# Optimization experiments

Measured on AMD Instinct MI355X. Metric: run time of the kernel, lower is better.

## Reference

```python
import jax, jax.numpy as jnp
import numpy as np

IN_F = 4096
OUT_F = 4096
PACKED_IN = IN_F // 16  # 16 ternary values per int32 (2 bits each)
TOKENS = 8192


def _pack(vals_int32):
    # vals_int32: [out, packed_in, 16] with entries in {0,1,2}
    shifts = (jnp.arange(16, dtype=jnp.int32) * 2)
    return jnp.sum(vals_int32 << shifts, axis=-1).astype(jnp.int32)


def _unpack_weight(packed, scale, in_features):
    # packed: [out, packed_in] int32 -> fp32 weight [out, in_features]
    shifts = (jnp.arange(16, dtype=jnp.int32) * 2)
    vals = (packed[:, :, None] >> shifts) & 3           # [out, packed_in, 16]
    w = vals.reshape(packed.shape[0], -1)[:, :in_features]
    return (w.astype(jnp.float32) - 1.0) * scale


def setup_inputs() -> dict:
    key = jax.random.key(0)
    k1, k2 = jax.random.split(key)
    x = jax.random.normal(k1, (TOKENS, IN_F), dtype=jnp.float32)
    # mapped ternary values in {0,1,2} (i.e. w_ternary + 1), packed 2-bit
    mapped = jax.random.randint(k2, (OUT_F, PACKED_IN, 16), 0, 3, dtype=jnp.int32)
    packed_weight = _pack(mapped)
    scale = jnp.float32(0.02)
    return {"x": x, "packed_weight": packed_weight, "scale": scale}


def reference(x, packed_weight, scale):
    # dequantize ternary weight
    w = _unpack_weight(packed_weight, scale, IN_F)      # [out, in]
    # abs-max activation scaling along the last dim
    x_scale = jnp.clip(jnp.max(jnp.abs(x), axis=-1, keepdims=True), 1e-5, None)
    x_scaled = x / x_scale
    out = jnp.einsum('ti,oi->to', x_scaled, w)          # F.linear (no bias)
    return out * x_scale
```

## Files before the change

### kernel.cpp

```cpp
#include <hip/hip_runtime.h>
#include <math.h>

typedef __attribute__((ext_vector_type(4)))  int   i32x4;
typedef __attribute__((ext_vector_type(16))) int   i32x16;
typedef __attribute__((ext_vector_type(4)))  float f32x4;

namespace {
constexpr int IN_F   = 4096;
constexpr int OUT_F  = 4096;
constexpr int TOKENS = 8192;
constexpr int PACKED = IN_F / 16;

constexpr int BM   = 256;
constexpr int BN   = 256;
constexpr int BK   = 128;
constexpr int NTHR = 512;
constexpr int NT   = IN_F / BK;

constexpr size_t XQ_BYTES = (size_t)TOKENS * IN_F;
constexpr size_t XS_BYTES = (size_t)TOKENS * 4;
constexpr size_t BQ_OFF   = XQ_BYTES + XS_BYTES;
constexpr size_t BQ_BYTES = (size_t)PACKED * OUT_F * 16;
constexpr size_t WS_NEED  = BQ_OFF + BQ_BYTES;
}

__device__ __forceinline__ i32x4 unpack16(unsigned w) {
  i32x4 r;
#pragma unroll
  for (int g = 0; g < 4; ++g) {
    unsigned t = (w >> (8 * g)) & 0xFFu;
    unsigned s = (t | (t << 6) | (t << 12) | (t << 18)) & 0x03030303u;
    r[g] = (int)((((s | 0x80808080u) - 0x01010101u) ^ 0x80808080u));
  }
  return r;
}

__global__ __launch_bounds__(256)
void prep(const float* __restrict__ X, signed char* __restrict__ XQ,
          float* __restrict__ XS, const unsigned* __restrict__ PW,
          signed char* __restrict__ BQ) {
  if (blockIdx.x < TOKENS / 4) {
    const int row  = blockIdx.x * 4 + (threadIdx.x >> 6);
    const int lane = threadIdx.x & 63;
    const float* xr = X + (size_t)row * IN_F;

    f32x4 v[16];
    float m = 0.f;
#pragma unroll
    for (int c = 0; c < 16; ++c) {
      v[c] = *(const f32x4*)(xr + c * 256 + lane * 4);
      m = fmaxf(m, fmaxf(fmaxf(fabsf(v[c].x), fabsf(v[c].y)),
                         fmaxf(fabsf(v[c].z), fabsf(v[c].w))));
    }
#pragma unroll
    for (int off = 32; off; off >>= 1) m = fmaxf(m, __shfl_xor(m, off, 64));
    m = fmaxf(m, 1e-5f);
    const float r = 127.f / m;

#pragma unroll
    for (int c = 0; c < 16; ++c) {
      int q0 = (int)rintf(v[c].x * r);
      int q1 = (int)rintf(v[c].y * r);
      int q2 = (int)rintf(v[c].z * r);
      int q3 = (int)rintf(v[c].w * r);
      unsigned d = (q0 & 255) | ((q1 & 255) << 8) | ((q2 & 255) << 16) | ((q3 & 255) << 24);
      *(unsigned*)(XQ + (size_t)row * IN_F + c * 256 + lane * 4) = d;
    }
    if (lane == 0) XS[row] = m;
  } else {
    const int g = (blockIdx.x - TOKENS / 4) * 256 + threadIdx.x;
    const int c = g >> 12;
    const int n = g & 4095;
    i32x4 u = unpack16(PW[(size_t)n * PACKED + c]);
    *(i32x4*)(BQ + ((size_t)c * OUT_F + n) * 16) = u;
  }
}


#define STAGE_A(BUF_, KT_)                                                      \
  {                                                                             \
    _Pragma("unroll")                                                           \
    for (int rb = 0; rb < 4; ++rb) {                                            \
      const signed char* src =                                                  \
          XQ + (size_t)(m0 + rb * 64 + lane) * IN_F + (KT_) * BK + w * 16;      \
      signed char* dst = lA + (BUF_) * 32768 + w * 4096 + rb * 1024;            \
      __builtin_amdgcn_global_load_lds(                                         \
          (const __attribute__((address_space(1))) void*)src,                   \
          (__attribute__((address_space(3))) void*)dst, 16, 0, 0);              \
    }                                                                           \
  }

#define STAGE_B(BUF_, KT_)                                                      \
  {                                                                             \
    _Pragma("unroll")                                                           \
    for (int j = 0; j < 4; ++j) {                                               \
      const signed char* src =                                                  \
          BQ + ((size_t)((KT_) * 8 + w) * OUT_F + n0 + j * 64 + lane) * 16;     \
      signed char* dst = lB + (BUF_) * 32768 + w * 4096 + j * 1024;             \
      __builtin_amdgcn_global_load_lds(                                         \
          (const __attribute__((address_space(1))) void*)src,                   \
          (__attribute__((address_space(3))) void*)dst, 16, 0, 0);              \
    }                                                                           \
  }

#define PHASE(KS_, BUF_)                                                        \
  {                                                                             \
    i32x4 afr[4], bfr[2];                                                       \
    _Pragma("unroll")                                                           \
    for (int mf = 0; mf < 4; ++mf)                                              \
      afr[mf] = *(const i32x4*)(lA + (BUF_) * 32768 + ((KS_) * 2 + h) * 4096 +  \
                                (wm * 128 + mf * 32 + l31) * 16);               \
    _Pragma("unroll")                                                           \
    for (int nf = 0; nf < 2; ++nf)                                              \
      bfr[nf] = *(const i32x4*)(lB + (BUF_) * 32768 + ((KS_) * 2 + h) * 4096 +  \
                                (wn * 64 + nf * 32 + l31) * 16);                \
    __builtin_amdgcn_s_setprio(1);                                              \
    _Pragma("unroll")                                                           \
    for (int mf = 0; mf < 4; ++mf) {                                            \
      acc[mf][0] = __builtin_amdgcn_mfma_i32_32x32x32_i8(afr[mf], bfr[0],       \
                                                         acc[mf][0], 0, 0, 0);  \
      acc[mf][1] = __builtin_amdgcn_mfma_i32_32x32x32_i8(afr[mf], bfr[1],       \
                                                         acc[mf][1], 0, 0, 0);  \
    }                                                                           \
    __builtin_amdgcn_s_setprio(0);                                              \
  }

#define TILE(KT_, CUR_, NXT_, PF_)                                              \
  {                                                                             \
    if (PF_) STAGE_A(NXT_, (KT_) + 1);                                          \
    PHASE(0, CUR_)                                                              \
    if (PF_) STAGE_B(NXT_, (KT_) + 1);                                          \
    PHASE(1, CUR_)                                                              \
    PHASE(2, CUR_)                                                              \
    PHASE(3, CUR_)                                                              \
    asm volatile("s_waitcnt vmcnt(0)" ::: "memory");                            \
    __builtin_amdgcn_s_barrier();                                               \
  }

__global__ __launch_bounds__(NTHR, 2)
void gemm_i8(const signed char* __restrict__ XQ, const signed char* __restrict__ BQ,
             const float* __restrict__ XS, const float* __restrict__ SC,
             float* __restrict__ OUT) {
  __shared__ signed char lA[2 * 32768];
  __shared__ signed char lB[2 * 32768];

  const int tid  = threadIdx.x;
  const int lane = tid & 63;
  const int w    = tid >> 6;
  const int wm   = w >> 2;
  const int wn   = w & 3;
  const int l31  = lane & 31;
  const int h    = lane >> 5;

  const int orig = blockIdx.y * gridDim.x + blockIdx.x;
  const int xcd  = orig & 7;
  const int idx  = orig >> 3;
  const int m0   = (idx >> 1) * BM;
  const int n0   = (xcd * 2 + (idx & 1)) * BN;

  i32x16 acc[4][2];
#pragma unroll
  for (int mf = 0; mf < 4; ++mf)
#pragma unroll
    for (int nf = 0; nf < 2; ++nf)
      acc[mf][nf] = (i32x16)(0);

  STAGE_A(0, 0);
  STAGE_B(0, 0);
  asm volatile("s_waitcnt vmcnt(0)" ::: "memory");
  __builtin_amdgcn_s_barrier();

  for (int kt = 0; kt < NT - 2; kt += 2) {
    TILE(kt,     0, 1, true);
    TILE(kt + 1, 1, 0, true);
  }
  TILE(NT - 2, 0, 1, true);
  TILE(NT - 1, 1, 0, false);

  const float sc = SC[0] / 127.f;
#pragma unroll
  for (int mf = 0; mf < 4; ++mf) {
    float fs[16];
#pragma unroll
    for (int r = 0; r < 16; ++r) {
      const int mm = m0 + wm * 128 + mf * 32 + 4 * h + (r & 3) + 8 * (r >> 2);
      fs[r] = sc * XS[mm];
    }
#pragma unroll
    for (int nf = 0; nf < 2; ++nf) {
      const int ncol = n0 + wn * 64 + nf * 32 + l31;
#pragma unroll
      for (int r = 0; r < 16; ++r) {
        const int mm = m0 + wm * 128 + mf * 32 + 4 * h + (r & 3) + 8 * (r >> 2);
        OUT[(size_t)mm * OUT_F + ncol] = (float)acc[mf][nf][r] * fs[r];
      }
    }
  }
}

__global__ __launch_bounds__(256, 2)
void gemm_i8_pw(const signed char* __restrict__ XQ, const unsigned* __restrict__ PW,
                const float* __restrict__ XS, const float* __restrict__ SC,
                float* __restrict__ OUT) {
  __shared__ signed char lA[256 * 128];

  const int tid  = threadIdx.x;
  const int lane = tid & 63;
  const int w    = tid >> 6;
  const int wm   = w >> 1;
  const int wn   = w & 1;
  const int l31  = lane & 31;
  const int h    = lane >> 5;

  const int m0 = blockIdx.y * 256;
  const int n0 = blockIdx.x * 128;

  i32x16 acc[4][2];
#pragma unroll
  for (int mf = 0; mf < 4; ++mf)
#pragma unroll
    for (int nf = 0; nf < 2; ++nf)
      acc[mf][nf] = (i32x16)(0);

  const unsigned* pb0 = PW + (size_t)(n0 + wn * 64 + 0 * 32 + l31) * PACKED;
  const unsigned* pb1 = PW + (size_t)(n0 + wn * 64 + 1 * 32 + l31) * PACKED;

  for (int kt = 0; kt < IN_F / 128; ++kt) {
#pragma unroll
    for (int cc = 0; cc < 2; ++cc) {
      const int c = w * 2 + cc;
#pragma unroll
      for (int rb = 0; rb < 4; ++rb) {
        const signed char* src =
            XQ + (size_t)(m0 + rb * 64 + lane) * IN_F + kt * 128 + c * 16;
        signed char* dst = lA + c * 4096 + rb * 1024;
        __builtin_amdgcn_global_load_lds(
            (const __attribute__((address_space(1))) void*)src,
            (__attribute__((address_space(3))) void*)dst, 16, 0, 0);
      }
    }

    unsigned bw0[4], bw1[4];
#pragma unroll
    for (int ks = 0; ks < 4; ++ks) {
      bw0[ks] = pb0[kt * 8 + ks * 2 + h];
      bw1[ks] = pb1[kt * 8 + ks * 2 + h];
    }

    __syncthreads();

#pragma unroll
    for (int ks = 0; ks < 4; ++ks) {
      i32x4 bfr0 = unpack16(bw0[ks]);
      i32x4 bfr1 = unpack16(bw1[ks]);
      i32x4 afr[4];
#pragma unroll
      for (int mf = 0; mf < 4; ++mf)
        afr[mf] = *(const i32x4*)(lA + (ks * 2 + h) * 4096 +
                                  (wm * 128 + mf * 32 + l31) * 16);
#pragma unroll
      for (int mf = 0; mf < 4; ++mf) {
        acc[mf][0] = __builtin_amdgcn_mfma_i32_32x32x32_i8(afr[mf], bfr0, acc[mf][0], 0, 0, 0);
        acc[mf][1] = __builtin_amdgcn_mfma_i32_32x32x32_i8(afr[mf], bfr1, acc[mf][1], 0, 0, 0);
      }
    }
    __syncthreads();
  }

  const float sc = SC[0] / 127.f;
#pragma unroll
  for (int mf = 0; mf < 4; ++mf) {
    float fs[16];
#pragma unroll
    for (int r = 0; r < 16; ++r) {
      const int mm = m0 + wm * 128 + mf * 32 + 4 * h + (r & 3) + 8 * (r >> 2);
      fs[r] = sc * XS[mm];
    }
#pragma unroll
    for (int nf = 0; nf < 2; ++nf) {
      const int ncol = n0 + wn * 64 + nf * 32 + l31;
#pragma unroll
      for (int r = 0; r < 16; ++r) {
        const int mm = m0 + wm * 128 + mf * 32 + 4 * h + (r & 3) + 8 * (r >> 2);
        OUT[(size_t)mm * OUT_F + ncol] = (float)acc[mf][nf][r] * fs[r];
      }
    }
  }
}

extern "C" void kernel_launch(void* const* d_in, const int* in_sizes, int n_in,
                              void* d_out, int out_size, void* d_ws, size_t ws_size,
                              hipStream_t stream) {
  const float*    x  = (const float*)d_in[0];
  const unsigned* pw = (const unsigned*)d_in[1];
  const float*    sc = (const float*)d_in[2];
  float*          out = (float*)d_out;

  signed char* xq = (signed char*)d_ws;
  float*       xs = (float*)((char*)d_ws + XQ_BYTES);

  if (ws_size >= WS_NEED) {
    signed char* bq = (signed char*)d_ws + BQ_OFF;
    prep<<<dim3(TOKENS / 4 + OUT_F * PACKED / 256), dim3(256), 0, stream>>>(
        x, xq, xs, pw, bq);
    dim3 grid(OUT_F / BN, TOKENS / BM);
    gemm_i8<<<grid, dim3(NTHR), 0, stream>>>(xq, bq, xs, sc, out);
  } else {
    prep<<<dim3(TOKENS / 4), dim3(256), 0, stream>>>(x, xq, xs, pw, nullptr);
    dim3 grid(OUT_F / 128, TOKENS / 256);
    gemm_i8_pw<<<grid, dim3(256), 0, stream>>>(xq, pw, xs, sc, out);
  }
}
```

Before: 397.0 us.

## Switch int8 GEMM to triple-buffered LDS pipeline with BK=64

Halves the K tile to 64 and replaces the double-buffered LDS scheme with three rotating buffers, prefetching two tiles ahead and waiting only on the older tile's loads via vmcnt(4). The aim is to keep more global-to-LDS traffic in flight and hide memory latency behind the MFMA work. Occupancy hint drops from 2 to 1 block per CU. The trade-off is twice as many barriers per K and less work per barrier interval.

```diff
diff --git a/kernel.cpp b/kernel.cpp
--- a/kernel.cpp
+++ b/kernel.cpp
@@ -13,7 +13,7 @@
 
 constexpr int BM   = 256;
 constexpr int BN   = 256;
-constexpr int BK   = 128;
+constexpr int BK   = 64;
 constexpr int NTHR = 512;
 constexpr int NT   = IN_F / BK;
 
@@ -77,42 +77,44 @@
 }
 
 
-#define STAGE_A(BUF_, KT_)                                                      \
+#define STAGE_A(BUFO_, KT_)                                                     \
   {                                                                             \
     _Pragma("unroll")                                                           \
-    for (int rb = 0; rb < 4; ++rb) {                                            \
+    for (int j = 0; j < 2; ++j) {                                               \
+      const int idx  = tid + j * 512;            \
       const signed char* src =                                                  \
-          XQ + (size_t)(m0 + rb * 64 + lane) * IN_F + (KT_) * BK + w * 16;      \
-      signed char* dst = lA + (BUF_) * 32768 + w * 4096 + rb * 1024;            \
+          XQ + (size_t)(m0 + (idx & 255)) * IN_F + (KT_) * BK + (idx >> 8) * 16;\
+      signed char* dst = lA + (BUFO_) + (w * 64 + j * 512) * 16;                \
       __builtin_amdgcn_global_load_lds(                                         \
           (const __attribute__((address_space(1))) void*)src,                   \
           (__attribute__((address_space(3))) void*)dst, 16, 0, 0);              \
     }                                                                           \
   }
 
-#define STAGE_B(BUF_, KT_)                                                      \
+#define STAGE_B(BUFO_, KT_)                                                     \
   {                                                                             \
     _Pragma("unroll")                                                           \
-    for (int j = 0; j < 4; ++j) {                                               \
-      const signed char* src =                                                  \
-          BQ + ((size_t)((KT_) * 8 + w) * OUT_F + n0 + j * 64 + lane) * 16;     \
-      signed char* dst = lB + (BUF_) * 32768 + w * 4096 + j * 1024;             \
+    for (int j = 0; j < 2; ++j) {                                               \
+      const int idx  = tid + j * 512;                                           \
+      const signed char* src = BQ +                                             \
+          ((size_t)((KT_) * 4 + (idx >> 8)) * OUT_F + n0 + (idx & 255)) * 16;   \
+      signed char* dst = lB + (BUFO_) + (w * 64 + j * 512) * 16;                \
       __builtin_amdgcn_global_load_lds(                                         \
           (const __attribute__((address_space(1))) void*)src,                   \
           (__attribute__((address_space(3))) void*)dst, 16, 0, 0);              \
     }                                                                           \
   }
 
-#define PHASE(KS_, BUF_)                                                        \
+#define KSTEP(KS_, BUFO_)                                                       \
   {                                                                             \
     i32x4 afr[4], bfr[2];                                                       \
     _Pragma("unroll")                                                           \
     for (int mf = 0; mf < 4; ++mf)                                              \
-      afr[mf] = *(const i32x4*)(lA + (BUF_) * 32768 + ((KS_) * 2 + h) * 4096 +  \
+      afr[mf] = *(const i32x4*)(lA + (BUFO_) + ((KS_) * 2 + h) * 4096 +         \
                                 (wm * 128 + mf * 32 + l31) * 16);               \
     _Pragma("unroll")                                                           \
     for (int nf = 0; nf < 2; ++nf)                                              \
-      bfr[nf] = *(const i32x4*)(lB + (BUF_) * 32768 + ((KS_) * 2 + h) * 4096 +  \
+      bfr[nf] = *(const i32x4*)(lB + (BUFO_) + ((KS_) * 2 + h) * 4096 +         \
                                 (wn * 64 + nf * 32 + l31) * 16);                \
     __builtin_amdgcn_s_setprio(1);                                              \
     _Pragma("unroll")                                                           \
@@ -125,24 +127,12 @@
     __builtin_amdgcn_s_setprio(0);                                              \
   }
 
-#define TILE(KT_, CUR_, NXT_, PF_)                                              \
-  {                                                                             \
-    if (PF_) STAGE_A(NXT_, (KT_) + 1);                                          \
-    PHASE(0, CUR_)                                                              \
-    if (PF_) STAGE_B(NXT_, (KT_) + 1);                                          \
-    PHASE(1, CUR_)                                                              \
-    PHASE(2, CUR_)                                                              \
-    PHASE(3, CUR_)                                                              \
-    asm volatile("s_waitcnt vmcnt(0)" ::: "memory");                            \
-    __builtin_amdgcn_s_barrier();                                               \
-  }
-
-__global__ __launch_bounds__(NTHR, 2)
+__global__ __launch_bounds__(NTHR, 1)
 void gemm_i8(const signed char* __restrict__ XQ, const signed char* __restrict__ BQ,
              const float* __restrict__ XS, const float* __restrict__ SC,
              float* __restrict__ OUT) {
-  __shared__ signed char lA[2 * 32768];
-  __shared__ signed char lB[2 * 32768];
+  __shared__ signed char lA[3 * 16384];
+  __shared__ signed char lB[3 * 16384];
 
   const int tid  = threadIdx.x;
   const int lane = tid & 63;
@@ -165,17 +155,31 @@
     for (int nf = 0; nf < 2; ++nf)
       acc[mf][nf] = (i32x16)(0);
 
-  STAGE_A(0, 0);
-  STAGE_B(0, 0);
-  asm volatile("s_waitcnt vmcnt(0)" ::: "memory");
+  int cur = 0, nxt = 16384, stg = 32768;
+
+  STAGE_A(cur, 0);
+  STAGE_B(cur, 0);
+  STAGE_A(nxt, 1);
+  STAGE_B(nxt, 1);
+  asm volatile("s_waitcnt vmcnt(4)" ::: "memory");
   __builtin_amdgcn_s_barrier();
 
-  for (int kt = 0; kt < NT - 2; kt += 2) {
-    TILE(kt,     0, 1, true);
-    TILE(kt + 1, 1, 0, true);
-  }
-  TILE(NT - 2, 0, 1, true);
-  TILE(NT - 1, 1, 0, false);
+  for (int kt = 0; kt < NT; ++kt) {
+    const bool st = (kt + 2 < NT);
+    if (st) {
+      STAGE_A(stg, kt + 2);
+      STAGE_B(stg, kt + 2);
+    }
+    KSTEP(0, cur)
+    KSTEP(1, cur)
+    if (st) {
+      asm volatile("s_waitcnt vmcnt(4)" ::: "memory");
+    } else {
+      asm volatile("s_waitcnt vmcnt(0)" ::: "memory");
+    }
+    __builtin_amdgcn_s_barrier();
+    const int t = cur; cur = nxt; nxt = stg; stg = t;
+  }
 
   const float sc = SC[0] / 127.f;
 #pragma unroll
```

Result: slower. 432.5 us (+8.9%).
